# Kernel tuning notes

Measured on AMD Instinct MI355X. Metric: run time of the kernel, lower is better.

## Reference

```python
import jax, jax.numpy as jnp
import numpy as np


def _gru(x, W, U, return_sequences):
    """Keras GRU, reset_after=True, recurrent_activation=sigmoid, activation=linear, no bias.
    x: [B,T,D], W: [D,3D] input kernel, U: [D,3D] recurrent kernel."""
    D = U.shape[0]
    xW = jnp.einsum('btd,de->bte', x, W)  # precompute input projections [B,T,3D]

    def step(h, xw_t):
        hu = h @ U  # [B,3D]
        xz, xr, xh = jnp.split(xw_t, 3, axis=-1)
        uz, ur, uh = jnp.split(hu, 3, axis=-1)
        z = jax.nn.sigmoid(xz + uz)          # update gate
        r = jax.nn.sigmoid(xr + ur)          # reset gate
        hh = xh + r * uh                     # candidate, linear activation, reset_after=True
        h_new = z * h + (1.0 - z) * hh
        return h_new, h_new

    h0 = jnp.zeros((x.shape[0], D), dtype=x.dtype)
    hT, hs = jax.lax.scan(step, h0, jnp.swapaxes(xW, 0, 1))  # scan over time
    return jnp.swapaxes(hs, 0, 1) if return_sequences else hT


def setup_inputs() -> dict:
    key = jax.random.key(0)
    ks = jax.random.split(key, 6)
    B, T, D = 16384, 25, 128
    s = 0.05  # keep gate pre-activations in a sane range
    return {
        "x": jax.random.normal(ks[0], (B, T, D), jnp.float32),
        "W1": jax.random.normal(ks[1], (D, 3 * D), jnp.float32) * s,
        "U1": jax.random.normal(ks[2], (D, 3 * D), jnp.float32) * s,
        "W2": jax.random.normal(ks[3], (D, 3 * D), jnp.float32) * s,
        "U2": jax.random.normal(ks[4], (D, 3 * D), jnp.float32) * s,
        "Wout": jax.random.normal(ks[5], (D, D), jnp.float32) * s,
    }


def reference(x, W1, U1, W2, U2, Wout):
    h1 = _gru(x, W1, U1, True)    # [B,T,D]
    h2 = _gru(h1, W2, U2, False)  # [B,D] last state
    return h2 @ Wout              # [B,D]
```

## Files before the change

### kernel.cpp

```cpp
#include <hip/hip_runtime.h>


typedef _Float16 half8 __attribute__((ext_vector_type(8)));
typedef __fp16  fp16x2 __attribute__((ext_vector_type(2)));
typedef float f32x4 __attribute__((ext_vector_type(4)));

#define MFMA(a, b, c) __builtin_amdgcn_mfma_f32_16x16x32_f16((a), (b), (c), 0, 0, 0)

constexpr int T_STEPS = 25;
constexpr int D = 128;
constexpr int NG = 384;
constexpr int BT = 64;
constexpr int SH = 136;
constexpr int SX = 132;

typedef const __attribute__((address_space(1))) unsigned int guint;
typedef __attribute__((address_space(3))) unsigned int luint;

__device__ __forceinline__ void load_lds4(const float* g, float* l) {
    __builtin_amdgcn_global_load_lds((guint*)(uintptr_t)g, (luint*)l, 4, 0, 0);
}

__device__ __forceinline__ float sigm(float v) { return 1.0f / (1.0f + __expf(-v)); }

__global__ __launch_bounds__(512, 2) void gru2_kernel(
    const float* __restrict__ x, const float* __restrict__ W1,
    const float* __restrict__ U1, const float* __restrict__ W2,
    const float* __restrict__ U2, const float* __restrict__ Wout,
    float* __restrict__ out) {
    __shared__ float    X[2][BT * SX];
    __shared__ _Float16 H1[2][BT * SH];
    __shared__ _Float16 H2[2][BT * SH];

    const int tid = threadIdx.x;
    const int w = tid >> 6, lane = tid & 63, l15 = lane & 15, quad = lane >> 4;
    const bool L2w = (w >= 4);
    const int wl = w & 3;
    const int b0 = blockIdx.x * BT;

    half8 wg[2][3][8];
    {
        const float* Wp = L2w ? W2 : W1;
        const float* Up = L2w ? U2 : U1;
#pragma unroll
        for (int j = 0; j < 2; ++j) {
            const int col0 = (2 * wl + j) * 16 + l15;
#pragma unroll
            for (int g = 0; g < 3; ++g) {
                const int c = g * 128 + col0;
#pragma unroll
                for (int k = 0; k < 8; ++k) {
                    const float* src = (k < 4 ? Wp : Up) + (size_t)((k & 3) * 32 + quad * 8) * NG + c;
                    half8 f;
#pragma unroll
                    for (int e = 0; e < 8; ++e) f[e] = (_Float16)src[(size_t)e * NG];
                    wg[j][g][k] = f;
                }
            }
        }
    }
#pragma unroll
    for (int j = 0; j < 2; ++j)
#pragma unroll
        for (int g = 0; g < 3; ++g)
#pragma unroll
            for (int k = 0; k < 8; ++k)
                asm volatile("" : "+a"(wg[j][g][k]));

    for (int idx = tid; idx < BT * SH; idx += 512) {
        H1[0][idx] = (_Float16)0.f;
        H2[1][idx] = (_Float16)0.f;
    }

#pragma unroll
    for (int r8 = 0; r8 < 16; ++r8) {
        const int idx = w * 16 + r8, row = idx >> 1, half = (idx & 1) * 64;
        load_lds4(x + ((size_t)(b0 + row) * T_STEPS + 0) * D + half + lane,
                  &X[0][row * SX + half]);
    }

    half8 hpv[2][2] = {};

    __syncthreads();

#pragma unroll 1
    for (int it = 0; it <= T_STEPS; ++it) {
        const int p = it & 1, q = p ^ 1;
        if (it + 1 < T_STEPS) {
#pragma unroll
            for (int r8 = 0; r8 < 16; ++r8) {
                const int idx = w * 16 + r8, row = idx >> 1, half = (idx & 1) * 64;
                load_lds4(x + ((size_t)(b0 + row) * T_STEPS + (it + 1)) * D + half + lane,
                          &X[q][row * SX + half]);
            }
        }
        const bool active = L2w ? (it >= 1) : (it < T_STEPS);
        if (active) {
            const _Float16* Hst = L2w ? H2[p] : H1[p];
            _Float16* Hout      = L2w ? H2[q] : H1[q];
            const _Float16* Hin = H1[p];
            const float* Xin    = X[p];
#pragma unroll
            for (int m = 0; m < 4; ++m) {
                const int arow = m * 16 + l15;
                half8 Ax[4], As[4];
                if (!L2w) {
                    const float* ap = Xin + arow * SX + quad * 8;
#pragma unroll
                    for (int k = 0; k < 4; ++k) {
                        const float4 v0 = *(const float4*)(ap + k * 32);
                        const float4 v1 = *(const float4*)(ap + k * 32 + 4);
                        union { fp16x2 h2[4]; half8 h8; } u;
                        u.h2[0] = __builtin_amdgcn_cvt_pkrtz(v0.x, v0.y);
                        u.h2[1] = __builtin_amdgcn_cvt_pkrtz(v0.z, v0.w);
                        u.h2[2] = __builtin_amdgcn_cvt_pkrtz(v1.x, v1.y);
                        u.h2[3] = __builtin_amdgcn_cvt_pkrtz(v1.z, v1.w);
                        Ax[k] = u.h8;
                    }
                } else {
                    const _Float16* ap = Hin + arow * SH + quad * 8;
#pragma unroll
                    for (int k = 0; k < 4; ++k) Ax[k] = *(const half8*)(ap + k * 32);
                }
                {
                    const _Float16* ap = Hst + arow * SH + quad * 8;
#pragma unroll
                    for (int k = 0; k < 4; ++k) As[k] = *(const half8*)(ap + k * 32);
                }
#pragma unroll
                for (int j = 0; j < 2; ++j) {
                    f32x4 cz = {0.f, 0.f, 0.f, 0.f}, cr = {0.f, 0.f, 0.f, 0.f};
                    f32x4 cxh = {0.f, 0.f, 0.f, 0.f}, cuh = {0.f, 0.f, 0.f, 0.f};
#pragma unroll
                    for (int k = 0; k < 4; ++k) {
                        cz  = MFMA(Ax[k], wg[j][0][k], cz);
                        cr  = MFMA(Ax[k], wg[j][1][k], cr);
                        cxh = MFMA(Ax[k], wg[j][2][k], cxh);
                    }
#pragma unroll
                    for (int k = 0; k < 4; ++k) {
                        cz  = MFMA(As[k], wg[j][0][4 + k], cz);
                        cr  = MFMA(As[k], wg[j][1][4 + k], cr);
                        cuh = MFMA(As[k], wg[j][2][4 + k], cuh);
                    }
                    const int d = (2 * wl + j) * 16 + l15;
#pragma unroll
                    for (int i2 = 0; i2 < 4; ++i2) {
                        const int el = m * 4 + i2;
                        const float hp = (float)hpv[j][el >> 3][el & 7];
                        const float z = sigm(cz[i2]);
                        const float r = sigm(cr[i2]);
                        const float hh = cxh[i2] + r * cuh[i2];
                        const float hn = hh + z * (hp - hh);
                        const _Float16 h16 = (_Float16)hn;
                        hpv[j][el >> 3][el & 7] = h16;
                        Hout[(m * 16 + quad * 4 + i2) * SH + d] = h16;
                    }
                }
            }
        }
        __syncthreads();
    }

    half8 wO[4];
    {
        const int col = w * 16 + l15;
#pragma unroll
        for (int k = 0; k < 4; ++k) {
            half8 f;
#pragma unroll
            for (int e = 0; e < 8; ++e)
                f[e] = (_Float16)Wout[(size_t)(k * 32 + quad * 8 + e) * D + col];
            wO[k] = f;
        }
    }
#pragma unroll
    for (int m = 0; m < 4; ++m) {
        half8 A[4];
        const _Float16* ap = H2[0] + (m * 16 + l15) * SH + quad * 8;
#pragma unroll
        for (int k = 0; k < 4; ++k) A[k] = *(const half8*)(ap + k * 32);
        f32x4 acc = {0.f, 0.f, 0.f, 0.f};
#pragma unroll
        for (int k = 0; k < 4; ++k) acc = MFMA(A[k], wO[k], acc);
        const int col = w * 16 + l15;
#pragma unroll
        for (int i2 = 0; i2 < 4; ++i2)
            out[(size_t)(b0 + m * 16 + quad * 4 + i2) * D + col] = acc[i2];
    }
}

extern "C" void kernel_launch(void* const* d_in, const int* in_sizes, int n_in,
                              void* d_out, int out_size, void* d_ws, size_t ws_size,
                              hipStream_t stream) {
    const float* x    = (const float*)d_in[0];
    const float* W1   = (const float*)d_in[1];
    const float* U1   = (const float*)d_in[2];
    const float* W2   = (const float*)d_in[3];
    const float* U2   = (const float*)d_in[4];
    const float* Wout = (const float*)d_in[5];
    gru2_kernel<<<dim3(16384 / BT), dim3(512), 0, stream>>>(
        x, W1, U1, W2, U2, Wout, (float*)d_out);
}
```

Before: 536.9 us.

## Use 1024-thread blocks with one 16-column slice per wave

Blocks grow from 512 to 1024 threads. Each wave now owns a single 16-column output slice of one layer, which halves the weight fragments held in registers and removes the AGPR pinning asm. The previous hidden state is re-read from LDS instead of being kept in registers, and the sigmoid uses a hardware reciprocal. The aim is more waves in flight per CU to hide MFMA and LDS latency. In exchange there is extra LDS traffic for the previous state, and the A-operand LDS reads are repeated across twice as many waves.

```diff
diff --git a/kernel.cpp b/kernel.cpp
--- a/kernel.cpp
+++ b/kernel.cpp
@@ -21,9 +21,11 @@
     __builtin_amdgcn_global_load_lds((guint*)(uintptr_t)g, (luint*)l, 4, 0, 0);
 }
 
-__device__ __forceinline__ float sigm(float v) { return 1.0f / (1.0f + __expf(-v)); }
+__device__ __forceinline__ float sigm(float v) {
+    return __builtin_amdgcn_rcpf(1.0f + __expf(-v));
+}
 
-__global__ __launch_bounds__(512, 2) void gru2_kernel(
+__global__ __launch_bounds__(1024, 4) void gru2_kernel(
     const float* __restrict__ x, const float* __restrict__ W1,
     const float* __restrict__ U1, const float* __restrict__ W2,
     const float* __restrict__ U2, const float* __restrict__ Wout,
@@ -34,52 +36,39 @@
 
     const int tid = threadIdx.x;
     const int w = tid >> 6, lane = tid & 63, l15 = lane & 15, quad = lane >> 4;
-    const bool L2w = (w >= 4);
-    const int wl = w & 3;
+    const int layer = w >> 3;
+    const int d0 = (w & 7) * 16;
     const int b0 = blockIdx.x * BT;
 
-    half8 wg[2][3][8];
+    half8 wg[3][8];
     {
-        const float* Wp = L2w ? W2 : W1;
-        const float* Up = L2w ? U2 : U1;
+        const float* Wp = layer ? W2 : W1;
+        const float* Up = layer ? U2 : U1;
 #pragma unroll
-        for (int j = 0; j < 2; ++j) {
-            const int col0 = (2 * wl + j) * 16 + l15;
+        for (int g = 0; g < 3; ++g) {
+            const int c = g * 128 + d0 + l15;
 #pragma unroll
-            for (int g = 0; g < 3; ++g) {
-                const int c = g * 128 + col0;
+            for (int k = 0; k < 8; ++k) {
+                const float* src = (k < 4 ? Wp : Up) + (size_t)((k & 3) * 32 + quad * 8) * NG + c;
+                half8 f;
 #pragma unroll
-                for (int k = 0; k < 8; ++k) {
-                    const float* src = (k < 4 ? Wp : Up) + (size_t)((k & 3) * 32 + quad * 8) * NG + c;
-                    half8 f;
-#pragma unroll
-                    for (int e = 0; e < 8; ++e) f[e] = (_Float16)src[(size_t)e * NG];
-                    wg[j][g][k] = f;
-                }
+                for (int e = 0; e < 8; ++e) f[e] = (_Float16)src[(size_t)e * NG];
+                wg[g][k] = f;
             }
         }
     }
-#pragma unroll
-    for (int j = 0; j < 2; ++j)
-#pragma unroll
-        for (int g = 0; g < 3; ++g)
-#pragma unroll
-            for (int k = 0; k < 8; ++k)
-                asm volatile("" : "+a"(wg[j][g][k]));
 
-    for (int idx = tid; idx < BT * SH; idx += 512) {
+    for (int idx = tid; idx < BT * SH; idx += 1024) {
         H1[0][idx] = (_Float16)0.f;
         H2[1][idx] = (_Float16)0.f;
     }
 
 #pragma unroll
-    for (int r8 = 0; r8 < 16; ++r8) {
-        const int idx = w * 16 + r8, row = idx >> 1, half = (idx & 1) * 64;
-        load_lds4(x + ((size_t)(b0 + row) * T_STEPS + 0) * D + half + lane,
-                  &X[0][row * SX + half]);
+    for (int r8 = 0; r8 < 8; ++r8) {
+        const int idx = w * 8 + r8, row = idx >> 1, hf = (idx & 1) * 64;
+        load_lds4(x + ((size_t)(b0 + row) * T_STEPS + 0) * D + hf + lane,
+                  &X[0][row * SX + hf]);
     }
-
-    half8 hpv[2][2] = {};
 
     __syncthreads();
 
@@ -88,83 +77,68 @@
         const int p = it & 1, q = p ^ 1;
         if (it + 1 < T_STEPS) {
 #pragma unroll
-            for (int r8 = 0; r8 < 16; ++r8) {
-                const int idx = w * 16 + r8, row = idx >> 1, half = (idx & 1) * 64;
-                load_lds4(x + ((size_t)(b0 + row) * T_STEPS + (it + 1)) * D + half + lane,
-                          &X[q][row * SX + half]);
+            for (int r8 = 0; r8 < 8; ++r8) {
+                const int idx = w * 8 + r8, row = idx >> 1, hf = (idx & 1) * 64;
+                load_lds4(x + ((size_t)(b0 + row) * T_STEPS + (it + 1)) * D + hf + lane,
+                          &X[q][row * SX + hf]);
             }
         }
-        const bool active = L2w ? (it >= 1) : (it < T_STEPS);
+        const bool active = layer ? (it >= 1) : (it < T_STEPS);
         if (active) {
-            const _Float16* Hst = L2w ? H2[p] : H1[p];
-            _Float16* Hout      = L2w ? H2[q] : H1[q];
+            const _Float16* Hst = layer ? H2[p] : H1[p];
+            _Float16* Hout      = layer ? H2[q] : H1[q];
             const _Float16* Hin = H1[p];
             const float* Xin    = X[p];
 #pragma unroll
             for (int m = 0; m < 4; ++m) {
                 const int arow = m * 16 + l15;
-                half8 Ax[4], As[4];
-                if (!L2w) {
-                    const float* ap = Xin + arow * SX + quad * 8;
+                f32x4 cz = {0.f, 0.f, 0.f, 0.f}, cr = {0.f, 0.f, 0.f, 0.f};
+                f32x4 cxh = {0.f, 0.f, 0.f, 0.f}, cuh = {0.f, 0.f, 0.f, 0.f};
 #pragma unroll
-                    for (int k = 0; k < 4; ++k) {
-                        const float4 v0 = *(const float4*)(ap + k * 32);
-                        const float4 v1 = *(const float4*)(ap + k * 32 + 4);
+                for (int k = 0; k < 4; ++k) {
+                    half8 A;
+                    if (!layer) {
+                        const float* ap = Xin + arow * SX + quad * 8 + k * 32;
+                        const float4 v0 = *(const float4*)(ap);
+                        const float4 v1 = *(const float4*)(ap + 4);
                         union { fp16x2 h2[4]; half8 h8; } u;
                         u.h2[0] = __builtin_amdgcn_cvt_pkrtz(v0.x, v0.y);
                         u.h2[1] = __builtin_amdgcn_cvt_pkrtz(v0.z, v0.w);
                         u.h2[2] = __builtin_amdgcn_cvt_pkrtz(v1.x, v1.y);
                         u.h2[3] = __builtin_amdgcn_cvt_pkrtz(v1.z, v1.w);
-                        Ax[k] = u.h8;
+                        A = u.h8;
+                    } else {
+                        A = *(const half8*)(Hin + arow * SH + quad * 8 + k * 32);
                     }
-                } else {
-                    const _Float16* ap = Hin + arow * SH + quad * 8;
-#pragma unroll
-                    for (int k = 0; k < 4; ++k) Ax[k] = *(const half8*)(ap + k * 32);
-                }
-                {
-                    const _Float16* ap = Hst + arow * SH + quad * 8;
-#pragma unroll
-                    for (int k = 0; k < 4; ++k) As[k] = *(const half8*)(ap + k * 32);
+                    cz  = MFMA(A, wg[0][k], cz);
+                    cr  = MFMA(A, wg[1][k], cr);
+                    cxh = MFMA(A, wg[2][k], cxh);
                 }
 #pragma unroll
-                for (int j = 0; j < 2; ++j) {
-                    f32x4 cz = {0.f, 0.f, 0.f, 0.f}, cr = {0.f, 0.f, 0.f, 0.f};
-                    f32x4 cxh = {0.f, 0.f, 0.f, 0.f}, cuh = {0.f, 0.f, 0.f, 0.f};
+                for (int k = 0; k < 4; ++k) {
+                    const half8 A = *(const half8*)(Hst + arow * SH + quad * 8 + k * 32);
+                    cz  = MFMA(A, wg[0][4 + k], cz);
+                    cr  = MFMA(A, wg[1][4 + k], cr);
+                    cuh = MFMA(A, wg[2][4 + k], cuh);
+                }
 #pragma unroll
-                    for (int k = 0; k < 4; ++k) {
-                        cz  = MFMA(Ax[k], wg[j][0][k], cz);
-                        cr  = MFMA(Ax[k], wg[j][1][k], cr);
-                        cxh = MFMA(Ax[k], wg[j][2][k], cxh);
-                    }
-#pragma unroll
-                    for (int k = 0; k < 4; ++k) {
-                        cz  = MFMA(As[k], wg[j][0][4 + k], cz);
-                        cr  = MFMA(As[k], wg[j][1][4 + k], cr);
-                        cuh = MFMA(As[k], wg[j][2][4 + k], cuh);
-                    }
-                    const int d = (2 * wl + j) * 16 + l15;
-#pragma unroll
-                    for (int i2 = 0; i2 < 4; ++i2) {
-                        const int el = m * 4 + i2;
-                        const float hp = (float)hpv[j][el >> 3][el & 7];
-                        const float z = sigm(cz[i2]);
-                        const float r = sigm(cr[i2]);
-                        const float hh = cxh[i2] + r * cuh[i2];
-                        const float hn = hh + z * (hp - hh);
-                        const _Float16 h16 = (_Float16)hn;
-                        hpv[j][el >> 3][el & 7] = h16;
-                        Hout[(m * 16 + quad * 4 + i2) * SH + d] = h16;
-                    }
+                for (int i2 = 0; i2 < 4; ++i2) {
+                    const int row = m * 16 + quad * 4 + i2;
+                    const float hp = (float)Hst[row * SH + d0 + l15];
+                    const float z = sigm(cz[i2]);
+                    const float r = sigm(cr[i2]);
+                    const float hh = cxh[i2] + r * cuh[i2];
+                    const float hn = hh + z * (hp - hh);
+                    Hout[row * SH + d0 + l15] = (_Float16)hn;
                 }
             }
         }
         __syncthreads();
     }
 
-    half8 wO[4];
-    {
-        const int col = w * 16 + l15;
+    if (layer) {
+        const int col = d0 + l15;
+        half8 wO[4];
 #pragma unroll
         for (int k = 0; k < 4; ++k) {
             half8 f;
@@ -173,20 +147,19 @@
                 f[e] = (_Float16)Wout[(size_t)(k * 32 + quad * 8 + e) * D + col];
             wO[k] = f;
         }
-    }
 #pragma unroll
-    for (int m = 0; m < 4; ++m) {
-        half8 A[4];
-        const _Float16* ap = H2[0] + (m * 16 + l15) * SH + quad * 8;
+        for (int m = 0; m < 4; ++m) {
+            const _Float16* ap = H2[0] + (m * 16 + l15) * SH + quad * 8;
+            f32x4 acc = {0.f, 0.f, 0.f, 0.f};
 #pragma unroll
-        for (int k = 0; k < 4; ++k) A[k] = *(const half8*)(ap + k * 32);
-        f32x4 acc = {0.f, 0.f, 0.f, 0.f};
+            for (int k = 0; k < 4; ++k) {
+                const half8 A = *(const half8*)(ap + k * 32);
+                acc = MFMA(A, wO[k], acc);
+            }
 #pragma unroll
-        for (int k = 0; k < 4; ++k) acc = MFMA(A[k], wO[k], acc);
-        const int col = w * 16 + l15;
-#pragma unroll
-        for (int i2 = 0; i2 < 4; ++i2)
-            out[(size_t)(b0 + m * 16 + quad * 4 + i2) * D + col] = acc[i2];
+            for (int i2 = 0; i2 < 4; ++i2)
+                out[(size_t)(b0 + m * 16 + quad * 4 + i2) * D + col] = acc[i2];
+        }
     }
 }
 
@@ -199,6 +172,6 @@
     const float* W2   = (const float*)d_in[3];
     const float* U2   = (const float*)d_in[4];
     const float* Wout = (const float*)d_in[5];
-    gru2_kernel<<<dim3(16384 / BT), dim3(512), 0, stream>>>(
+    gru2_kernel<<<dim3(16384 / BT), dim3(1024), 0, stream>>>(
         x, W1, U1, W2, U2, Wout, (float*)d_out);
 }
```

Result: faster. 514.4 us (-4.2%).
